# Optimization experiments

Measured on AMD Instinct MI355X. Metric: run time of the kernel, lower is better.

The kernel has to match this reference:

```python
import jax, jax.numpy as jnp
import numpy as np

P = 512        # n_predicates
C = 65536      # n_constants
L = 1          # max_rule_length (only runnable config of original code)


def setup_inputs() -> dict:
    key = jax.random.key(0)
    k1, k2 = jax.random.split(key)
    initial_facts = jax.random.uniform(k1, (P, C), dtype=jnp.float32)
    rule_weights = jax.random.normal(k2, (P, L, P), dtype=jnp.float32)
    return {"initial_facts": initial_facts, "rule_weights": rule_weights, "n_iterations": 3}


def reference(initial_facts, rule_weights, n_iterations):
    # F.softmax(rule[step], dim=0) on the 1-D vector rule_weights[r, 0, :]
    # == softmax over the last axis of rule_weights[:, 0, :].
    # Stacking apply_rule over all rules r is exactly A @ facts.
    A = jax.nn.softmax(rule_weights[:, 0, :], axis=-1)  # [P, P]
    facts = initial_facts                                # [P, C]
    for _ in range(n_iterations):
        derived = A @ facts                              # [P, C] (rule r -> row r)
        facts = jnp.maximum(facts, derived.max(axis=0))  # broadcast [C] over [P, C]
    return facts
```

## Files before the change

kernel.cpp:

```cpp
#include <hip/hip_runtime.h>
#include <hip/hip_bf16.h>
#include <cstdint>


typedef __attribute__((ext_vector_type(8))) short bf16x8;
typedef __attribute__((ext_vector_type(8))) unsigned short u16x8;
typedef __attribute__((ext_vector_type(16))) float f32x16;
typedef unsigned short ushort_t;
typedef unsigned int uint32;

#define PDIM 512
#define CDIM 65536
#define NT   128
#define WAVES 8

__device__ __forceinline__ ushort_t f2bf(float x) {
    uint32 u = __float_as_uint(x);
    return (ushort_t)((u + 0x7fffu + ((u >> 16) & 1u)) >> 16);
}
__device__ __forceinline__ float bf2f(uint32 bits) { return __uint_as_float(bits << 16); }

__device__ __forceinline__ bf16x8 pkmax8(bf16x8 v, ushort_t mu) {
    u16x8 a = __builtin_bit_cast(u16x8, v);
    const u16x8 mb = {mu, mu, mu, mu, mu, mu, mu, mu};
    a = __builtin_elementwise_max(a, mb);
    return __builtin_bit_cast(bf16x8, a);
}

__global__ __launch_bounds__(64) void softmax_pack(const float* __restrict__ rw,
                                                   ushort_t* __restrict__ Apk) {
    const int r  = blockIdx.x;
    const int ln = threadIdx.x;
    const float* row = rw + r * PDIM;
    float4 x0 = *(const float4*)(row + ln * 8);
    float4 x1 = *(const float4*)(row + ln * 8 + 4);
    float v[8] = {x0.x, x0.y, x0.z, x0.w, x1.x, x1.y, x1.z, x1.w};

    float mx = -1e30f;
    #pragma unroll
    for (int i = 0; i < 8; ++i) mx = fmaxf(mx, v[i]);
    #pragma unroll
    for (int d = 1; d < 64; d <<= 1) mx = fmaxf(mx, __shfl_xor(mx, d, 64));
    float s = 0.f;
    #pragma unroll
    for (int i = 0; i < 8; ++i) { v[i] = __expf(v[i] - mx); s += v[i]; }
    #pragma unroll
    for (int d = 1; d < 64; d <<= 1) s += __shfl_xor(s, d, 64);
    const float inv = 1.f / s;

    ushort_t o[8];
    #pragma unroll
    for (int i = 0; i < 8; ++i) o[i] = f2bf(v[i] * inv);
    const int idx16 = ((ln >> 1) * 16 + (r >> 5)) * 64 + ((ln & 1) << 5) + (r & 31);
    *(int4*)(Apk + idx16 * 8) = *(const int4*)o;
}

__global__ __launch_bounds__(512, 2) void ilp_kernel(
        const float* __restrict__ facts,
        const ushort_t* __restrict__ Apk,
        const int* __restrict__ n_iter_p,
        float* __restrict__ out) {
    __shared__ ushort_t ft[64 * NT * 8];
    __shared__ float wred[WAVES][NT];

    const int tid  = threadIdx.x;
    const int wave = tid >> 6;
    const int lane = tid & 63;
    const int l31  = lane & 31;
    const int half = lane >> 5;
    const int c0   = blockIdx.x * NT;

    int n_iter = *n_iter_p;
    n_iter = n_iter < 0 ? 0 : (n_iter > 8 ? 8 : n_iter);

    wred[wave][lane]      = 0.f;
    wred[wave][lane + 64] = 0.f;

    {
        const int c   = tid & 127;
        const int grp = tid >> 7;
        #pragma unroll 4
        for (int s = 0; s < 16; ++s) {
            const int g = grp * 16 + s;
            ushort_t gb[8];
            #pragma unroll
            for (int i = 0; i < 8; ++i)
                gb[i] = f2bf(facts[(g * 8 + i) * CDIM + c0 + c]);
            *(int4*)(&ft[(g * NT + c) * 8]) = *(const int4*)gb;
        }
    }

    const ushort_t* abase = Apk + wave * 1024 + (half * 32 + l31) * 8;
    bf16x8 aF[2][2], bR[2][4];
    aF[0][0] = *(const bf16x8*)(abase);
    aF[0][1] = *(const bf16x8*)(abase + 512);
    aF[1][0] = *(const bf16x8*)(abase + 8192);
    aF[1][1] = *(const bf16x8*)(abase + 8192 + 512);

    __syncthreads();

    const int bbase = (half * NT + l31) * 8;
    #pragma unroll
    for (int ct2 = 0; ct2 < 4; ++ct2) {
        bR[0][ct2] = *(const bf16x8*)(&ft[bbase + ct2 * 256]);
        bR[1][ct2] = *(const bf16x8*)(&ft[bbase + 2048 + ct2 * 256]);
    }

    #pragma unroll 1
    for (int it = 0; it < n_iter; ++it) {
        f32x16 acc[2][4];
        #pragma unroll
        for (int rt2 = 0; rt2 < 2; ++rt2)
            #pragma unroll
            for (int ct2 = 0; ct2 < 4; ++ct2)
                #pragma unroll
                for (int e = 0; e < 16; ++e) acc[rt2][ct2][e] = 0.f;

        #pragma unroll 2
        for (int kt2 = 0; kt2 < 32; ++kt2) {
            const int cur = kt2 & 1;

            __builtin_amdgcn_s_setprio(1);
            #pragma unroll
            for (int ct2 = 0; ct2 < 4; ++ct2) {
                acc[0][ct2] = __builtin_amdgcn_mfma_f32_32x32x16_bf16(
                    aF[cur][0], bR[cur][ct2], acc[0][ct2], 0, 0, 0);
                acc[1][ct2] = __builtin_amdgcn_mfma_f32_32x32x16_bf16(
                    aF[cur][1], bR[cur][ct2], acc[1][ct2], 0, 0, 0);
            }
            __builtin_amdgcn_s_setprio(0);

            const int ktp = (kt2 + 2) & 31;
            const ushort_t* ap = abase + ktp * 8192;
            aF[cur][0] = *(const bf16x8*)(ap);
            aF[cur][1] = *(const bf16x8*)(ap + 512);
            const int bo = bbase + ktp * 2048;
            #pragma unroll
            for (int ct2 = 0; ct2 < 4; ++ct2)
                bR[cur][ct2] = *(const bf16x8*)(&ft[bo + ct2 * 256]);
        }

        #pragma unroll
        for (int ct2 = 0; ct2 < 4; ++ct2) {
            float m0 = -1e30f;
            #pragma unroll
            for (int rt2 = 0; rt2 < 2; ++rt2)
                #pragma unroll
                for (int e = 0; e < 16; ++e) m0 = fmaxf(m0, acc[rt2][ct2][e]);
            m0 = fmaxf(m0, __shfl_xor(m0, 32, 64));
            if (half == 0) wred[wave][ct2 * 32 + l31] = m0;
        }
        __syncthreads();

        if (it < n_iter - 1) {
            const int c   = tid & 127;
            const int grp = tid >> 7;
            float m = wred[0][c];
            #pragma unroll
            for (int w = 1; w < WAVES; ++w) m = fmaxf(m, wred[w][c]);
            const ushort_t mu = f2bf(m);
            #pragma unroll
            for (int s = 0; s < 16; ++s) {
                const int idx = ((grp * 16 + s) * NT + c) * 8;
                bf16x8 v = *(const bf16x8*)(&ft[idx]);
                *(bf16x8*)(&ft[idx]) = pkmax8(v, mu);
            }
            __syncthreads();
            #pragma unroll
            for (int ct2 = 0; ct2 < 4; ++ct2) {
                bR[0][ct2] = *(const bf16x8*)(&ft[bbase + ct2 * 256]);
                bR[1][ct2] = *(const bf16x8*)(&ft[bbase + 2048 + ct2 * 256]);
            }
        }
    }

    {
        const int c   = tid & 127;
        const int grp = tid >> 7;
        float m = wred[0][c];
        #pragma unroll
        for (int w = 1; w < WAVES; ++w) m = fmaxf(m, wred[w][c]);
        #pragma unroll 4
        for (int s = 0; s < 16; ++s) {
            const int g = grp * 16 + s;
            ushort_t gb[8];
            *(int4*)gb = *(const int4*)(&ft[(g * NT + c) * 8]);
            #pragma unroll
            for (int i = 0; i < 8; ++i)
                out[(g * 8 + i) * CDIM + c0 + c] = fmaxf(bf2f(gb[i]), m);
        }
    }
}

extern "C" void kernel_launch(void* const* d_in, const int* in_sizes, int n_in,
                              void* d_out, int out_size, void* d_ws, size_t ws_size,
                              hipStream_t stream) {
    const float* facts    = (const float*)d_in[0];
    const float* rw       = (const float*)d_in[1];
    const int*   n_iter_p = (const int*)d_in[2];
    float* out = (float*)d_out;

    ushort_t* Apk = (ushort_t*)d_ws;

    softmax_pack<<<PDIM, 64, 0, stream>>>(rw, Apk);
    ilp_kernel<<<CDIM / NT, 512, 0, stream>>>(facts, Apk, n_iter_p, out);
}
```

Baseline: 308.2 us.

## Apply per-column max lazily to B fragments instead of rewriting LDS tile

Stops rewriting the whole bf16 facts tile in LDS between iterations. Each lane now keeps a running per-column max in registers and applies it with a packed max to each B fragment just before the MFMA. This removes one LDS read-modify-write pass and one barrier per iteration, and the reduction buffer is double-buffered so the remaining barrier is safe. It also fully unrolls the K loop with a three-slot register prefetch, drops the setprio hints, and preloads the first A fragments before the barrier, which raises register pressure and adds a few vector max ops per K step.

```diff
diff --git a/kernel.cpp b/kernel.cpp
--- a/kernel.cpp
+++ b/kernel.cpp
@@ -61,7 +61,7 @@
         const int* __restrict__ n_iter_p,
         float* __restrict__ out) {
     __shared__ ushort_t ft[64 * NT * 8];
-    __shared__ float wred[WAVES][NT];
+    __shared__ float wred[2][WAVES][NT];
 
     const int tid  = threadIdx.x;
     const int wave = tid >> 6;
@@ -73,8 +73,8 @@
     int n_iter = *n_iter_p;
     n_iter = n_iter < 0 ? 0 : (n_iter > 8 ? 8 : n_iter);
 
-    wred[wave][lane]      = 0.f;
-    wred[wave][lane + 64] = 0.f;
+    wred[0][wave][lane]      = 0.f;
+    wred[0][wave][lane + 64] = 0.f;
 
     {
         const int c   = tid & 127;
@@ -91,20 +91,24 @@
     }
 
     const ushort_t* abase = Apk + wave * 1024 + (half * 32 + l31) * 8;
-    bf16x8 aF[2][2], bR[2][4];
-    aF[0][0] = *(const bf16x8*)(abase);
-    aF[0][1] = *(const bf16x8*)(abase + 512);
-    aF[1][0] = *(const bf16x8*)(abase + 8192);
-    aF[1][1] = *(const bf16x8*)(abase + 8192 + 512);
+    bf16x8 aF[3][2], bR[3][4];
+    #pragma unroll
+    for (int s = 0; s < 2; ++s) {
+        aF[s][0] = *(const bf16x8*)(abase + s * 8192);
+        aF[s][1] = *(const bf16x8*)(abase + s * 8192 + 512);
+    }
 
     __syncthreads();
 
     const int bbase = (half * NT + l31) * 8;
     #pragma unroll
-    for (int ct2 = 0; ct2 < 4; ++ct2) {
-        bR[0][ct2] = *(const bf16x8*)(&ft[bbase + ct2 * 256]);
-        bR[1][ct2] = *(const bf16x8*)(&ft[bbase + 2048 + ct2 * 256]);
-    }
+    for (int s = 0; s < 2; ++s)
+        #pragma unroll
+        for (int ct2 = 0; ct2 < 4; ++ct2)
+            bR[s][ct2] = *(const bf16x8*)(&ft[bbase + s * 2048 + ct2 * 256]);
+
+    ushort_t ml[4] = {0, 0, 0, 0};
+    float    mf[4] = {0.f, 0.f, 0.f, 0.f};
 
     #pragma unroll 1
     for (int it = 0; it < n_iter; ++it) {
@@ -116,28 +120,36 @@
                 #pragma unroll
                 for (int e = 0; e < 16; ++e) acc[rt2][ct2][e] = 0.f;
 
-        #pragma unroll 2
+        #pragma unroll
         for (int kt2 = 0; kt2 < 32; ++kt2) {
-            const int cur = kt2 & 1;
-
-            __builtin_amdgcn_s_setprio(1);
+            const int cur = kt2 % 3;
+
+            if (kt2 < 30) {
+                const int nxt = (kt2 + 2) % 3;
+                {
+                    const int bo = bbase + (kt2 + 2) * 2048;
+                    #pragma unroll
+                    for (int ct2 = 0; ct2 < 4; ++ct2)
+                        bR[nxt][ct2] = *(const bf16x8*)(&ft[bo + ct2 * 256]);
+                }
+                {
+                    const ushort_t* ap = abase + (kt2 + 2) * 8192;
+                    aF[nxt][0] = *(const bf16x8*)(ap);
+                    aF[nxt][1] = *(const bf16x8*)(ap + 512);
+                }
+            }
+
+            bf16x8 bC[4];
+            #pragma unroll
+            for (int ct2 = 0; ct2 < 4; ++ct2) bC[ct2] = pkmax8(bR[cur][ct2], ml[ct2]);
+
             #pragma unroll
             for (int ct2 = 0; ct2 < 4; ++ct2) {
                 acc[0][ct2] = __builtin_amdgcn_mfma_f32_32x32x16_bf16(
-                    aF[cur][0], bR[cur][ct2], acc[0][ct2], 0, 0, 0);
+                    aF[cur][0], bC[ct2], acc[0][ct2], 0, 0, 0);
                 acc[1][ct2] = __builtin_amdgcn_mfma_f32_32x32x16_bf16(
-                    aF[cur][1], bR[cur][ct2], acc[1][ct2], 0, 0, 0);
+                    aF[cur][1], bC[ct2], acc[1][ct2], 0, 0, 0);
             }
-            __builtin_amdgcn_s_setprio(0);
-
-            const int ktp = (kt2 + 2) & 31;
-            const ushort_t* ap = abase + ktp * 8192;
-            aF[cur][0] = *(const bf16x8*)(ap);
-            aF[cur][1] = *(const bf16x8*)(ap + 512);
-            const int bo = bbase + ktp * 2048;
-            #pragma unroll
-            for (int ct2 = 0; ct2 < 4; ++ct2)
-                bR[cur][ct2] = *(const bf16x8*)(&ft[bo + ct2 * 256]);
         }
 
         #pragma unroll
@@ -148,38 +160,42 @@
                 #pragma unroll
                 for (int e = 0; e < 16; ++e) m0 = fmaxf(m0, acc[rt2][ct2][e]);
             m0 = fmaxf(m0, __shfl_xor(m0, 32, 64));
-            if (half == 0) wred[wave][ct2 * 32 + l31] = m0;
+            if (half == 0) wred[it & 1][wave][ct2 * 32 + l31] = m0;
+        }
+
+        if (it < n_iter - 1) {
+            #pragma unroll
+            for (int s = 0; s < 2; ++s) {
+                aF[s][0] = *(const bf16x8*)(abase + s * 8192);
+                aF[s][1] = *(const bf16x8*)(abase + s * 8192 + 512);
+            }
         }
         __syncthreads();
-
+        #pragma unroll
+        for (int ct2 = 0; ct2 < 4; ++ct2) {
+            const int c = ct2 * 32 + l31;
+            float m = wred[it & 1][0][c];
+            #pragma unroll
+            for (int w = 1; w < WAVES; ++w) m = fmaxf(m, wred[it & 1][w][c]);
+            mf[ct2] = fmaxf(mf[ct2], m);
+            ml[ct2] = f2bf(mf[ct2]);
+        }
         if (it < n_iter - 1) {
-            const int c   = tid & 127;
-            const int grp = tid >> 7;
-            float m = wred[0][c];
-            #pragma unroll
-            for (int w = 1; w < WAVES; ++w) m = fmaxf(m, wred[w][c]);
-            const ushort_t mu = f2bf(m);
-            #pragma unroll
-            for (int s = 0; s < 16; ++s) {
-                const int idx = ((grp * 16 + s) * NT + c) * 8;
-                bf16x8 v = *(const bf16x8*)(&ft[idx]);
-                *(bf16x8*)(&ft[idx]) = pkmax8(v, mu);
-            }
-            __syncthreads();
-            #pragma unroll
-            for (int ct2 = 0; ct2 < 4; ++ct2) {
-                bR[0][ct2] = *(const bf16x8*)(&ft[bbase + ct2 * 256]);
-                bR[1][ct2] = *(const bf16x8*)(&ft[bbase + 2048 + ct2 * 256]);
-            }
+            #pragma unroll
+            for (int s = 0; s < 2; ++s)
+                #pragma unroll
+                for (int ct2 = 0; ct2 < 4; ++ct2)
+                    bR[s][ct2] = *(const bf16x8*)(&ft[bbase + s * 2048 + ct2 * 256]);
         }
     }
 
     {
         const int c   = tid & 127;
         const int grp = tid >> 7;
-        float m = wred[0][c];
-        #pragma unroll
-        for (int w = 1; w < WAVES; ++w) m = fmaxf(m, wred[w][c]);
+        const int lb  = (n_iter > 0) ? ((n_iter - 1) & 1) : 0;
+        float m = wred[lb][0][c];
+        #pragma unroll
+        for (int w = 1; w < WAVES; ++w) m = fmaxf(m, wred[lb][w][c]);
         #pragma unroll 4
         for (int s = 0; s < 16; ++s) {
             const int g = grp * 16 + s;
```

New measurement: 369.2 us. +19.8%, slower.
